# Performance work log

Measured on AMD Instinct MI355X. Metric: run time of the kernel, lower is better.

The kernel has to match this reference:

```python
import jax, jax.numpy as jnp
import numpy as np

DIM = 1024
HEADS = 16
DIM_HEAD = 64
INNER = HEADS * DIM_HEAD  # 1024
SCALE = DIM ** (-0.5)     # NOTE: source uses dim, not dim_head, for scaling


def setup_inputs() -> dict:
    key = jax.random.key(0)
    k_x, k_qkv, k_out = jax.random.split(key, 3)
    x = jax.random.normal(k_x, (4, 2048, DIM), dtype=jnp.float32)
    # store weights pre-transposed: y = x @ W  (equivalent to torch Linear with W.T)
    w_qkv = jax.random.normal(k_qkv, (DIM, 3 * INNER), dtype=jnp.float32) * 0.02
    w_out = jax.random.normal(k_out, (INNER, DIM), dtype=jnp.float32) * 0.02
    b_out = jnp.zeros((DIM,), dtype=jnp.float32)
    return {"x": x, "w_qkv": w_qkv, "w_out": w_out, "b_out": b_out}


def reference(x, w_qkv, w_out, b_out):
    b, n, _ = x.shape
    qkv = x @ w_qkv                                  # [b, n, 3*inner]
    q, k, v = jnp.split(qkv, 3, axis=-1)             # each [b, n, inner]

    def to_heads(t):
        return t.reshape(b, n, HEADS, DIM_HEAD).transpose(0, 2, 1, 3)  # [b, h, n, d]

    q, k, v = to_heads(q), to_heads(k), to_heads(v)
    dots = jnp.einsum("bhid,bhjd->bhij", q, k) * SCALE   # [b, h, n, n]
    attn = jax.nn.softmax(dots, axis=-1)
    out = jnp.einsum("bhij,bhjd->bhid", attn, v)         # [b, h, n, d]
    out = out.transpose(0, 2, 1, 3).reshape(b, n, INNER)  # [b, n, inner]
    return out @ w_out + b_out                            # dropout p=0 -> identity
```

## Files before the change

### kernel.cpp

```cpp
#include <hip/hip_runtime.h>
#include <math.h>

#define BATCH   4
#define NSEQ    2048
#define DIM     1024
#define HEADS   16
#define DHEAD   64
#define INNER   1024
#define MTOT    (BATCH*NSEQ)
#define SC_L2E  0.04508422f

typedef __attribute__((ext_vector_type(8))) unsigned short u16x8;
typedef __attribute__((ext_vector_type(4))) unsigned short u16x4;
typedef __attribute__((ext_vector_type(8))) short          bf16x8;
typedef __attribute__((ext_vector_type(4))) float          f32x4;

__device__ __forceinline__ unsigned short f2bf(float f) {
    unsigned int u = __builtin_bit_cast(unsigned int, f);
    u += 0x7FFFu + ((u >> 16) & 1u);
    return (unsigned short)(u >> 16);
}

__device__ __forceinline__ float fexp2(float x) {
    float r; asm("v_exp_f32 %0, %1" : "=v"(r) : "v"(x)); return r;
}

__device__ __forceinline__ unsigned int cvtpk(float lo, float hi) {
    unsigned int r; asm("v_cvt_pk_bf16_f32 %0, %1, %2" : "=v"(r) : "v"(lo), "v"(hi));
    return r;
}

#define GLDS16(gp, lp) __builtin_amdgcn_global_load_lds( \
    (const __attribute__((address_space(1))) unsigned int*)(gp), \
    (__attribute__((address_space(3))) unsigned int*)(lp), 16, 0, 0)

#define SWC(r, c) ((c) ^ (((r) & 7) << 3))

__global__ __launch_bounds__(256) void cvt_bf16(const float* __restrict__ in,
                                                unsigned short* __restrict__ out)
{
    const int i = blockIdx.x * 256 + threadIdx.x;
    const float4* p = reinterpret_cast<const float4*>(in) + (size_t)i * 2;
    float4 a = p[0], b = p[1];
    u16x8 o;
    o[0]=f2bf(a.x); o[1]=f2bf(a.y); o[2]=f2bf(a.z); o[3]=f2bf(a.w);
    o[4]=f2bf(b.x); o[5]=f2bf(b.y); o[6]=f2bf(b.z); o[7]=f2bf(b.w);
    reinterpret_cast<u16x8*>(out)[i] = o;
}

__global__ __launch_bounds__(256) void transp_bf16(const float* __restrict__ in,
                                                   unsigned short* __restrict__ out,
                                                   int R, int C)
{
    __shared__ float tile[32][33];
    const int c0 = blockIdx.x * 32, r0 = blockIdx.y * 32;
    const int tx = threadIdx.x & 31, ty = threadIdx.x >> 5;
#pragma unroll
    for (int i = 0; i < 32; i += 8)
        tile[ty + i][tx] = in[(size_t)(r0 + ty + i) * C + c0 + tx];
    __syncthreads();
#pragma unroll
    for (int i = 0; i < 32; i += 8)
        out[(size_t)(c0 + ty + i) * R + r0 + tx] = f2bf(tile[tx][ty + i]);
}


__global__ __launch_bounds__(256) void gemm_qkv_mfma(const unsigned short* __restrict__ A,
                                                     const unsigned short* __restrict__ Bt,
                                                     unsigned short* __restrict__ qb,
                                                     unsigned short* __restrict__ kb,
                                                     unsigned short* __restrict__ vt)
{
    __shared__ unsigned short As[128][32];
    __shared__ unsigned short Bs[128][32];

    const int t = threadIdx.x;
    const int l = t & 63, w = t >> 6;
    const int wr = w >> 1, wc = w & 1;
    const int g = l >> 4, ql = l & 15;
    const int row0 = blockIdx.y * 128;
    const int col0 = blockIdx.x * 128;
    const int lr = l >> 2, lc = l & 3;

    f32x4 acc[4][4];
#pragma unroll
    for (int mi = 0; mi < 4; ++mi)
#pragma unroll
        for (int ni = 0; ni < 4; ++ni)
#pragma unroll
            for (int r = 0; r < 4; ++r) acc[mi][ni][r] = 0.f;

    for (int k0 = 0; k0 < DIM; k0 += 32) {
        __syncthreads();
        {
            const unsigned short* ag = A  + (size_t)(row0 + 32 * w + lr) * DIM + k0 + lc * 8;
            const unsigned short* bg = Bt + (size_t)(col0 + 32 * w + lr) * DIM + k0 + lc * 8;
            GLDS16(ag,              &As[32 * w][0]);
            GLDS16(ag + 16 * DIM,   &As[32 * w + 16][0]);
            GLDS16(bg,              &Bs[32 * w][0]);
            GLDS16(bg + 16 * DIM,   &Bs[32 * w + 16][0]);
        }
        __syncthreads();

        bf16x8 af[4], bf[4];
#pragma unroll
        for (int mi = 0; mi < 4; ++mi)
            af[mi] = *reinterpret_cast<const bf16x8*>(&As[wr * 64 + mi * 16 + ql][g * 8]);
#pragma unroll
        for (int ni = 0; ni < 4; ++ni)
            bf[ni] = *reinterpret_cast<const bf16x8*>(&Bs[wc * 64 + ni * 16 + ql][g * 8]);
#pragma unroll
        for (int mi = 0; mi < 4; ++mi)
#pragma unroll
            for (int ni = 0; ni < 4; ++ni)
                acc[mi][ni] = __builtin_amdgcn_mfma_f32_16x16x32_bf16(af[mi], bf[ni], acc[mi][ni], 0, 0, 0);
    }

#pragma unroll
    for (int mi = 0; mi < 4; ++mi) {
        const int m0 = row0 + wr * 64 + mi * 16 + g * 4;
        const int b  = m0 >> 11, n0 = m0 & 2047;
#pragma unroll
        for (int ni = 0; ni < 4; ++ni) {
            const int c = col0 + wc * 64 + ni * 16 + ql;
            const int part = c >> 10, inner = c & 1023;
            const int h = inner >> 6, d = inner & 63;
            if (part == 2) {
                const int key0 = n0 & 63;
                const int nst  = (n0 & ~63)
                               | (key0 & 0x23)
                               | (((key0 >> 3) & 1) << 4)
                               | (((key0 >> 2) & 1) << 3)
                               | (((key0 >> 4) & 1) << 2);
                u16x4 pk;
#pragma unroll
                for (int r = 0; r < 4; ++r) pk[r] = f2bf(acc[mi][ni][r]);
                *reinterpret_cast<u16x4*>(&vt[(((size_t)b * HEADS + h) * DHEAD + d) * NSEQ + nst]) = pk;
            } else if (part == 0) {
                unsigned short* dst = qb + (((size_t)b * HEADS + h) * NSEQ + n0) * DHEAD + d;
#pragma unroll
                for (int r = 0; r < 4; ++r) dst[(size_t)r * DHEAD] = f2bf(acc[mi][ni][r] * SC_L2E);
            } else {
                unsigned short* dst = kb + (((size_t)b * HEADS + h) * NSEQ + n0) * DHEAD + d;
#pragma unroll
                for (int r = 0; r < 4; ++r) dst[(size_t)r * DHEAD] = f2bf(acc[mi][ni][r]);
            }
        }
    }
}

__global__ __launch_bounds__(256) void gemm_out_mfma(const unsigned short* __restrict__ A,
                                                     const unsigned short* __restrict__ Bt,
                                                     const float* __restrict__ bias,
                                                     float* __restrict__ out)
{
    __shared__ unsigned short As[128][32];
    __shared__ unsigned short Bs[128][32];

    const int t = threadIdx.x;
    const int l = t & 63, w = t >> 6;
    const int wr = w >> 1, wc = w & 1;
    const int g = l >> 4, ql = l & 15;
    const int row0 = blockIdx.y * 128;
    const int col0 = blockIdx.x * 128;
    const int lr = l >> 2, lc = l & 3;

    f32x4 acc[4][4];
#pragma unroll
    for (int mi = 0; mi < 4; ++mi)
#pragma unroll
        for (int ni = 0; ni < 4; ++ni)
#pragma unroll
            for (int r = 0; r < 4; ++r) acc[mi][ni][r] = 0.f;

    for (int k0 = 0; k0 < INNER; k0 += 32) {
        __syncthreads();
        {
            const unsigned short* ag = A  + (size_t)(row0 + 32 * w + lr) * INNER + k0 + lc * 8;
            const unsigned short* bg = Bt + (size_t)(col0 + 32 * w + lr) * INNER + k0 + lc * 8;
            GLDS16(ag,               &As[32 * w][0]);
            GLDS16(ag + 16 * INNER,  &As[32 * w + 16][0]);
            GLDS16(bg,               &Bs[32 * w][0]);
            GLDS16(bg + 16 * INNER,  &Bs[32 * w + 16][0]);
        }
        __syncthreads();

        bf16x8 af[4], bf[4];
#pragma unroll
        for (int mi = 0; mi < 4; ++mi)
            af[mi] = *reinterpret_cast<const bf16x8*>(&As[wr * 64 + mi * 16 + ql][g * 8]);
#pragma unroll
        for (int ni = 0; ni < 4; ++ni)
            bf[ni] = *reinterpret_cast<const bf16x8*>(&Bs[wc * 64 + ni * 16 + ql][g * 8]);
#pragma unroll
        for (int mi = 0; mi < 4; ++mi)
#pragma unroll
            for (int ni = 0; ni < 4; ++ni)
                acc[mi][ni] = __builtin_amdgcn_mfma_f32_16x16x32_bf16(af[mi], bf[ni], acc[mi][ni], 0, 0, 0);
    }

#pragma unroll
    for (int mi = 0; mi < 4; ++mi) {
        const int m0 = row0 + wr * 64 + mi * 16 + g * 4;
#pragma unroll
        for (int ni = 0; ni < 4; ++ni) {
            const int c = col0 + wc * 64 + ni * 16 + ql;
            const float bv = bias[c];
#pragma unroll
            for (int r = 0; r < 4; ++r)
                out[(size_t)(m0 + r) * DIM + c] = acc[mi][ni][r] + bv;
        }
    }
}

__global__ __launch_bounds__(512) void attn_mfma(const unsigned short* __restrict__ qg,
                                                 const unsigned short* __restrict__ kg,
                                                 const unsigned short* __restrict__ vtg,
                                                 unsigned short* __restrict__ og)
{
    __shared__ unsigned short Ks [2][64 * 64];
    __shared__ unsigned short Vts[2][64 * 64];

    const int bh = blockIdx.x;
    const int b = bh >> 4, h = bh & 15;
    const int qblk = blockIdx.y;
    const int t = threadIdx.x, l = t & 63, w = t >> 6;
    const int g = l >> 4, ql = l & 15;

    const size_t hb = (size_t)bh * NSEQ * DHEAD;

    bf16x8 qf[2][2];
#pragma unroll
    for (int qh = 0; qh < 2; ++qh) {
        const unsigned short* qrow = qg + hb + (size_t)(qblk * 256 + w * 32 + qh * 16 + ql) * DHEAD;
        qf[qh][0] = *reinterpret_cast<const bf16x8*>(qrow + g * 8);
        qf[qh][1] = *reinterpret_cast<const bf16x8*>(qrow + 32 + g * 8);
    }

    const int r = t >> 3, seg = t & 7;
    const unsigned short* kgp = kg  + hb + (size_t)r * DHEAD + seg * 8;
    const unsigned short* vgp = vtg + hb + (size_t)r * NSEQ  + seg * 8;
    const int st = r * 64 + ((seg ^ (r & 7)) * 8);

    {
        u16x8 k0 = *reinterpret_cast<const u16x8*>(kgp);
        u16x8 v0 = *reinterpret_cast<const u16x8*>(vgp);
        *reinterpret_cast<u16x8*>(&Ks [0][st]) = k0;
        *reinterpret_cast<u16x8*>(&Vts[0][st]) = v0;
    }
    __syncthreads();

    const unsigned short* kpre = kgp + 64 * DHEAD;
    const unsigned short* vpre = vgp + 64;

    f32x4 acc_o[2][4];
#pragma unroll
    for (int qh = 0; qh < 2; ++qh)
#pragma unroll
        for (int dt = 0; dt < 4; ++dt)
#pragma unroll
            for (int rr = 0; rr < 4; ++rr) acc_o[qh][dt][rr] = 0.f;
    float m_r[2] = {-INFINITY, -INFINITY};
    float l_r[2] = {0.f, 0.f};

    for (int kbi = 0; kbi < NSEQ / 64; ++kbi) {
        const int cur = kbi & 1;
        u16x8 nk, nv;
        const bool pre = (kbi + 1 < NSEQ / 64);
        if (pre) {
            nk = *reinterpret_cast<const u16x8*>(kpre);
            nv = *reinterpret_cast<const u16x8*>(vpre);
            kpre += 64 * DHEAD;
            vpre += 64;
        }

        f32x4 sacc[2][4];
#pragma unroll
        for (int qh = 0; qh < 2; ++qh)
#pragma unroll
            for (int jt = 0; jt < 4; ++jt)
#pragma unroll
                for (int rr = 0; rr < 4; ++rr) sacc[qh][jt][rr] = 0.f;
        __builtin_amdgcn_s_setprio(1);
#pragma unroll
        for (int jt = 0; jt < 4; ++jt) {
            const int row = jt * 16 + ql;
            bf16x8 kf0 = *reinterpret_cast<const bf16x8*>(&Ks[cur][row * 64 + SWC(row, g * 8)]);
            bf16x8 kf1 = *reinterpret_cast<const bf16x8*>(&Ks[cur][row * 64 + SWC(row, 32 + g * 8)]);
            sacc[0][jt] = __builtin_amdgcn_mfma_f32_16x16x32_bf16(kf0, qf[0][0], sacc[0][jt], 0, 0, 0);
            sacc[0][jt] = __builtin_amdgcn_mfma_f32_16x16x32_bf16(kf1, qf[0][1], sacc[0][jt], 0, 0, 0);
            sacc[1][jt] = __builtin_amdgcn_mfma_f32_16x16x32_bf16(kf0, qf[1][0], sacc[1][jt], 0, 0, 0);
            sacc[1][jt] = __builtin_amdgcn_mfma_f32_16x16x32_bf16(kf1, qf[1][1], sacc[1][jt], 0, 0, 0);
        }
        __builtin_amdgcn_s_setprio(0);

        bf16x8 pf[2][2];
#pragma unroll
        for (int qh = 0; qh < 2; ++qh) {
            float a0 = fmaxf(fmaxf(sacc[qh][0][0], sacc[qh][0][1]), sacc[qh][0][2]);
            float a1 = fmaxf(fmaxf(sacc[qh][0][3], sacc[qh][1][0]), sacc[qh][1][1]);
            float a2 = fmaxf(fmaxf(sacc[qh][1][2], sacc[qh][1][3]), sacc[qh][2][0]);
            float a3 = fmaxf(fmaxf(sacc[qh][2][1], sacc[qh][2][2]), sacc[qh][2][3]);
            float a4 = fmaxf(fmaxf(sacc[qh][3][0], sacc[qh][3][1]), sacc[qh][3][2]);
            float mx = fmaxf(fmaxf(fmaxf(a0, a1), a2), fmaxf(fmaxf(a3, a4), sacc[qh][3][3]));
            mx = fmaxf(mx, __shfl_xor(mx, 16));
            mx = fmaxf(mx, __shfl_xor(mx, 32));
            if (__any(mx > m_r[qh] + 8.f)) {
                const float m_new = fmaxf(m_r[qh], mx);
                const float alpha = fexp2(m_r[qh] - m_new);
                l_r[qh] *= alpha;
#pragma unroll
                for (int dt = 0; dt < 4; ++dt)
#pragma unroll
                    for (int rr = 0; rr < 4; ++rr) acc_o[qh][dt][rr] *= alpha;
                m_r[qh] = m_new;
            }
            float p[16];
#pragma unroll
            for (int jt = 0; jt < 4; ++jt)
#pragma unroll
                for (int rr = 0; rr < 4; ++rr)
                    p[jt * 4 + rr] = fexp2(sacc[qh][jt][rr] - m_r[qh]);
            float s0 = (p[0] + p[1]) + (p[2] + p[3]);
            float s1 = (p[4] + p[5]) + (p[6] + p[7]);
            float s2 = (p[8] + p[9]) + (p[10] + p[11]);
            float s3 = (p[12] + p[13]) + (p[14] + p[15]);
            float ps = (s0 + s1) + (s2 + s3);
            ps += __shfl_xor(ps, 16);
            ps += __shfl_xor(ps, 32);
            l_r[qh] += ps;

#pragma unroll
            for (int js = 0; js < 2; ++js) {
                unsigned int u0 = cvtpk(p[8 * js + 0], p[8 * js + 1]);
                unsigned int u1 = cvtpk(p[8 * js + 2], p[8 * js + 3]);
                unsigned int u2 = cvtpk(p[8 * js + 4], p[8 * js + 5]);
                unsigned int u3 = cvtpk(p[8 * js + 6], p[8 * js + 7]);
                uint4 uu = {u0, u1, u2, u3};
                pf[qh][js] = __builtin_bit_cast(bf16x8, uu);
            }
        }

        __builtin_amdgcn_s_setprio(1);
#pragma unroll
        for (int js = 0; js < 2; ++js) {
            bf16x8 vf[4];
#pragma unroll
            for (int dt = 0; dt < 4; ++dt) {
                const int row = dt * 16 + ql;
                vf[dt] = *reinterpret_cast<const bf16x8*>(&Vts[cur][row * 64 + SWC(row, js * 32 + g * 8)]);
            }
#pragma unroll
            for (int qh = 0; qh < 2; ++qh)
#pragma unroll
                for (int dt = 0; dt < 4; ++dt)
                    acc_o[qh][dt] = __builtin_amdgcn_mfma_f32_16x16x32_bf16(vf[dt], pf[qh][js], acc_o[qh][dt], 0, 0, 0);
        }
        __builtin_amdgcn_s_setprio(0);

        if (pre) {
            *reinterpret_cast<u16x8*>(&Ks [cur ^ 1][st]) = nk;
            *reinterpret_cast<u16x8*>(&Vts[cur ^ 1][st]) = nv;
        }
        __syncthreads();
    }

#pragma unroll
    for (int qh = 0; qh < 2; ++qh) {
        const float rinv = 1.0f / l_r[qh];
        const int n = qblk * 256 + w * 32 + qh * 16 + ql;
        unsigned short* dst = og + ((size_t)b * NSEQ + n) * INNER + h * DHEAD;
#pragma unroll
        for (int dt = 0; dt < 4; ++dt) {
            uint2 u;
            u.x = cvtpk(acc_o[qh][dt][0] * rinv, acc_o[qh][dt][1] * rinv);
            u.y = cvtpk(acc_o[qh][dt][2] * rinv, acc_o[qh][dt][3] * rinv);
            *reinterpret_cast<uint2*>(&dst[dt * 16 + g * 4]) = u;
        }
    }
}


extern "C" void kernel_launch(void* const* d_in, const int* in_sizes, int n_in,
                              void* d_out, int out_size, void* d_ws, size_t ws_size,
                              hipStream_t stream) {
    const float* x     = (const float*)d_in[0];
    const float* w_qkv = (const float*)d_in[1];
    const float* w_out = (const float*)d_in[2];
    const float* b_out = (const float*)d_in[3];
    float* out = (float*)d_out;

    unsigned short* ws = (unsigned short*)d_ws;
    const size_t nX  = (size_t)MTOT * DIM;
    const size_t nWq = (size_t)DIM * 3 * INNER;
    const size_t nWo = (size_t)DIM * INNER;
    unsigned short* Xb  = ws;
    unsigned short* Wqt = Xb  + nX;
    unsigned short* Wot = Wqt + nWq;
    unsigned short* qb  = Wot + nWo;
    unsigned short* kb  = qb  + nX;
    unsigned short* vt  = kb  + nX;
    unsigned short* Ob  = vt  + nX;

    cvt_bf16<<<dim3(nX / 8 / 256), dim3(256), 0, stream>>>(x, Xb);
    transp_bf16<<<dim3(3 * INNER / 32, DIM / 32), dim3(256), 0, stream>>>(w_qkv, Wqt, DIM, 3 * INNER);
    transp_bf16<<<dim3(DIM / 32, INNER / 32), dim3(256), 0, stream>>>(w_out, Wot, INNER, DIM);

    gemm_qkv_mfma<<<dim3(3 * INNER / 128, MTOT / 128), dim3(256), 0, stream>>>(Xb, Wqt, qb, kb, vt);
    attn_mfma<<<dim3(BATCH * HEADS, NSEQ / 256), dim3(512), 0, stream>>>(qb, kb, vt, Ob);
    gemm_out_mfma<<<dim3(DIM / 128, MTOT / 128), dim3(256), 0, stream>>>(Ob, Wot, b_out, out);
}
```

Baseline: 202.4 us.

## Rewrite QKV GEMM with 256x256 tiles, double-buffered LDS and phased MFMA scheduling

Replaces the 128x128 QKV projection GEMM with a 512-thread kernel that computes 256x256 output tiles over K-steps of 64. It double-buffers LDS, splits the next-tile global-to-LDS loads across the compute phases, and swizzles LDS addressing. MFMA bursts are wrapped in barriers with raised wave priority, a ping-pong style schedule meant to overlap memory traffic with matrix math and raise data reuse. The trade-offs are much larger LDS use (128 KB) and more accumulator registers, which lower occupancy. The grid also drops to 384 blocks, which may under-fill the GPU.

```diff
diff --git a/kernel.cpp b/kernel.cpp
--- a/kernel.cpp
+++ b/kernel.cpp
@@ -35,6 +35,8 @@
     (__attribute__((address_space(3))) unsigned int*)(lp), 16, 0, 0)
 
 #define SWC(r, c) ((c) ^ (((r) & 7) << 3))
+
+#define BAR() __builtin_amdgcn_s_barrier()
 
 __global__ __launch_bounds__(256) void cvt_bf16(const float* __restrict__ in,
                                                 unsigned short* __restrict__ out)
@@ -64,65 +66,177 @@
         out[(size_t)(c0 + ty + i) * R + r0 + tx] = f2bf(tile[tx][ty + i]);
 }
 
-
-__global__ __launch_bounds__(256) void gemm_qkv_mfma(const unsigned short* __restrict__ A,
-                                                     const unsigned short* __restrict__ Bt,
-                                                     unsigned short* __restrict__ qb,
-                                                     unsigned short* __restrict__ kb,
-                                                     unsigned short* __restrict__ vt)
+__global__ __launch_bounds__(512) void gemm_qkv_8p(const unsigned short* __restrict__ A,
+                                                   const unsigned short* __restrict__ Bt,
+                                                   unsigned short* __restrict__ qb,
+                                                   unsigned short* __restrict__ kb,
+                                                   unsigned short* __restrict__ vt)
 {
-    __shared__ unsigned short As[128][32];
-    __shared__ unsigned short Bs[128][32];
+    __shared__ unsigned short As[2][256 * 64];
+    __shared__ unsigned short Bs[2][256 * 64];
 
     const int t = threadIdx.x;
     const int l = t & 63, w = t >> 6;
-    const int wr = w >> 1, wc = w & 1;
+    const int wm = w >> 2, wn = w & 3;
     const int g = l >> 4, ql = l & 15;
-    const int row0 = blockIdx.y * 128;
-    const int col0 = blockIdx.x * 128;
-    const int lr = l >> 2, lc = l & 3;
-
-    f32x4 acc[4][4];
-#pragma unroll
-    for (int mi = 0; mi < 4; ++mi)
-#pragma unroll
-        for (int ni = 0; ni < 4; ++ni)
-#pragma unroll
-            for (int r = 0; r < 4; ++r) acc[mi][ni][r] = 0.f;
-
-    for (int k0 = 0; k0 < DIM; k0 += 32) {
-        __syncthreads();
+    const int row0 = blockIdx.y * 256;
+    const int col0 = blockIdx.x * 256;
+
+    const int lrow  = l >> 3;
+    const int lslot = (l & 7) ^ (lrow & 7);
+    const unsigned short* aSrc = A  + (size_t)(row0 + w * 32 + lrow) * DIM + lslot * 8;
+    const unsigned short* bSrc = Bt + (size_t)(col0 + w * 32 + lrow) * DIM + lslot * 8;
+
+    f32x4 acc[8][4];
+#pragma unroll
+    for (int mf = 0; mf < 8; ++mf)
+#pragma unroll
+        for (int nf = 0; nf < 4; ++nf)
+#pragma unroll
+            for (int r = 0; r < 4; ++r) acc[mf][nf][r] = 0.f;
+
+#pragma unroll
+    for (int i = 0; i < 4; ++i) {
+        GLDS16(aSrc + (size_t)i * 8 * DIM, &As[0][(w * 32 + i * 8) * 64]);
+        GLDS16(bSrc + (size_t)i * 8 * DIM, &Bs[0][(w * 32 + i * 8) * 64]);
+    }
+    asm volatile("s_waitcnt vmcnt(0)" ::: "memory");
+    __syncthreads();
+
+#pragma unroll 1
+    for (int kt = 0; kt < 16; ++kt) {
+        const int cur = kt & 1;
+        const int nxt = cur ^ 1;
+        const size_t nk0 = (size_t)(kt + 1) * 64;
+        const bool pre = (kt < 15);
+
+        bf16x8 bfc[4][2];
+
+        if (pre) {
+            GLDS16(aSrc + nk0,                   &As[nxt][(w * 32) * 64]);
+            GLDS16(aSrc + nk0 + (size_t)8 * DIM, &As[nxt][(w * 32 + 8) * 64]);
+            GLDS16(bSrc + nk0,                   &Bs[nxt][(w * 32) * 64]);
+            GLDS16(bSrc + nk0 + (size_t)8 * DIM, &Bs[nxt][(w * 32 + 8) * 64]);
+        }
+#pragma unroll
+        for (int nf = 0; nf < 4; ++nf) {
+            const int br = wn * 64 + nf * 16 + ql;
+#pragma unroll
+            for (int kh = 0; kh < 2; ++kh)
+                bfc[nf][kh] = *reinterpret_cast<const bf16x8*>(
+                    &Bs[cur][br * 64 + SWC(br, (kh * 4 + g) * 8)]);
+        }
         {
-            const unsigned short* ag = A  + (size_t)(row0 + 32 * w + lr) * DIM + k0 + lc * 8;
-            const unsigned short* bg = Bt + (size_t)(col0 + 32 * w + lr) * DIM + k0 + lc * 8;
-            GLDS16(ag,              &As[32 * w][0]);
-            GLDS16(ag + 16 * DIM,   &As[32 * w + 16][0]);
-            GLDS16(bg,              &Bs[32 * w][0]);
-            GLDS16(bg + 16 * DIM,   &Bs[32 * w + 16][0]);
-        }
-        __syncthreads();
-
-        bf16x8 af[4], bf[4];
-#pragma unroll
-        for (int mi = 0; mi < 4; ++mi)
-            af[mi] = *reinterpret_cast<const bf16x8*>(&As[wr * 64 + mi * 16 + ql][g * 8]);
-#pragma unroll
-        for (int ni = 0; ni < 4; ++ni)
-            bf[ni] = *reinterpret_cast<const bf16x8*>(&Bs[wc * 64 + ni * 16 + ql][g * 8]);
-#pragma unroll
-        for (int mi = 0; mi < 4; ++mi)
-#pragma unroll
-            for (int ni = 0; ni < 4; ++ni)
-                acc[mi][ni] = __builtin_amdgcn_mfma_f32_16x16x32_bf16(af[mi], bf[ni], acc[mi][ni], 0, 0, 0);
-    }
-
-#pragma unroll
-    for (int mi = 0; mi < 4; ++mi) {
-        const int m0 = row0 + wr * 64 + mi * 16 + g * 4;
+            bf16x8 af[2][2];
+#pragma unroll
+            for (int j = 0; j < 2; ++j) {
+                const int ar = wm * 128 + (0 + j) * 16 + ql;
+#pragma unroll
+                for (int kh = 0; kh < 2; ++kh)
+                    af[j][kh] = *reinterpret_cast<const bf16x8*>(
+                        &As[cur][ar * 64 + SWC(ar, (kh * 4 + g) * 8)]);
+            }
+            BAR();
+            __builtin_amdgcn_s_setprio(1);
+#pragma unroll
+            for (int j = 0; j < 2; ++j)
+#pragma unroll
+                for (int nf = 0; nf < 4; ++nf)
+#pragma unroll
+                    for (int kh = 0; kh < 2; ++kh)
+                        acc[0 + j][nf] = __builtin_amdgcn_mfma_f32_16x16x32_bf16(
+                            af[j][kh], bfc[nf][kh], acc[0 + j][nf], 0, 0, 0);
+            __builtin_amdgcn_s_setprio(0);
+            BAR();
+        }
+
+        if (pre) {
+            GLDS16(aSrc + nk0 + (size_t)16 * DIM, &As[nxt][(w * 32 + 16) * 64]);
+            GLDS16(aSrc + nk0 + (size_t)24 * DIM, &As[nxt][(w * 32 + 24) * 64]);
+            GLDS16(bSrc + nk0 + (size_t)16 * DIM, &Bs[nxt][(w * 32 + 16) * 64]);
+            GLDS16(bSrc + nk0 + (size_t)24 * DIM, &Bs[nxt][(w * 32 + 24) * 64]);
+        }
+        {
+            bf16x8 af[2][2];
+#pragma unroll
+            for (int j = 0; j < 2; ++j) {
+                const int ar = wm * 128 + (2 + j) * 16 + ql;
+#pragma unroll
+                for (int kh = 0; kh < 2; ++kh)
+                    af[j][kh] = *reinterpret_cast<const bf16x8*>(
+                        &As[cur][ar * 64 + SWC(ar, (kh * 4 + g) * 8)]);
+            }
+            BAR();
+            __builtin_amdgcn_s_setprio(1);
+#pragma unroll
+            for (int j = 0; j < 2; ++j)
+#pragma unroll
+                for (int nf = 0; nf < 4; ++nf)
+#pragma unroll
+                    for (int kh = 0; kh < 2; ++kh)
+                        acc[2 + j][nf] = __builtin_amdgcn_mfma_f32_16x16x32_bf16(
+                            af[j][kh], bfc[nf][kh], acc[2 + j][nf], 0, 0, 0);
+            __builtin_amdgcn_s_setprio(0);
+            BAR();
+        }
+
+        {
+            bf16x8 af[2][2];
+#pragma unroll
+            for (int j = 0; j < 2; ++j) {
+                const int ar = wm * 128 + (4 + j) * 16 + ql;
+#pragma unroll
+                for (int kh = 0; kh < 2; ++kh)
+                    af[j][kh] = *reinterpret_cast<const bf16x8*>(
+                        &As[cur][ar * 64 + SWC(ar, (kh * 4 + g) * 8)]);
+            }
+            BAR();
+            __builtin_amdgcn_s_setprio(1);
+#pragma unroll
+            for (int j = 0; j < 2; ++j)
+#pragma unroll
+                for (int nf = 0; nf < 4; ++nf)
+#pragma unroll
+                    for (int kh = 0; kh < 2; ++kh)
+                        acc[4 + j][nf] = __builtin_amdgcn_mfma_f32_16x16x32_bf16(
+                            af[j][kh], bfc[nf][kh], acc[4 + j][nf], 0, 0, 0);
+            __builtin_amdgcn_s_setprio(0);
+            BAR();
+        }
+
+        {
+            bf16x8 af[2][2];
+#pragma unroll
+            for (int j = 0; j < 2; ++j) {
+                const int ar = wm * 128 + (6 + j) * 16 + ql;
+#pragma unroll
+                for (int kh = 0; kh < 2; ++kh)
+                    af[j][kh] = *reinterpret_cast<const bf16x8*>(
+                        &As[cur][ar * 64 + SWC(ar, (kh * 4 + g) * 8)]);
+            }
+            BAR();
+            __builtin_amdgcn_s_setprio(1);
+#pragma unroll
+            for (int j = 0; j < 2; ++j)
+#pragma unroll
+                for (int nf = 0; nf < 4; ++nf)
+#pragma unroll
+                    for (int kh = 0; kh < 2; ++kh)
+                        acc[6 + j][nf] = __builtin_amdgcn_mfma_f32_16x16x32_bf16(
+                            af[j][kh], bfc[nf][kh], acc[6 + j][nf], 0, 0, 0);
+            __builtin_amdgcn_s_setprio(0);
+            asm volatile("s_waitcnt vmcnt(0)" ::: "memory");
+            BAR();
+        }
+    }
+
+#pragma unroll
+    for (int mf = 0; mf < 8; ++mf) {
+        const int m0 = row0 + wm * 128 + mf * 16 + g * 4;
         const int b  = m0 >> 11, n0 = m0 & 2047;
 #pragma unroll
-        for (int ni = 0; ni < 4; ++ni) {
-            const int c = col0 + wc * 64 + ni * 16 + ql;
+        for (int nf = 0; nf < 4; ++nf) {
+            const int c = col0 + wn * 64 + nf * 16 + ql;
             const int part = c >> 10, inner = c & 1023;
             const int h = inner >> 6, d = inner & 63;
             if (part == 2) {
@@ -134,16 +248,16 @@
                                | (((key0 >> 4) & 1) << 2);
                 u16x4 pk;
 #pragma unroll
-                for (int r = 0; r < 4; ++r) pk[r] = f2bf(acc[mi][ni][r]);
+                for (int r = 0; r < 4; ++r) pk[r] = f2bf(acc[mf][nf][r]);
                 *reinterpret_cast<u16x4*>(&vt[(((size_t)b * HEADS + h) * DHEAD + d) * NSEQ + nst]) = pk;
             } else if (part == 0) {
                 unsigned short* dst = qb + (((size_t)b * HEADS + h) * NSEQ + n0) * DHEAD + d;
 #pragma unroll
-                for (int r = 0; r < 4; ++r) dst[(size_t)r * DHEAD] = f2bf(acc[mi][ni][r] * SC_L2E);
+                for (int r = 0; r < 4; ++r) dst[(size_t)r * DHEAD] = f2bf(acc[mf][nf][r] * SC_L2E);
             } else {
                 unsigned short* dst = kb + (((size_t)b * HEADS + h) * NSEQ + n0) * DHEAD + d;
 #pragma unroll
-                for (int r = 0; r < 4; ++r) dst[(size_t)r * DHEAD] = f2bf(acc[mi][ni][r]);
+                for (int r = 0; r < 4; ++r) dst[(size_t)r * DHEAD] = f2bf(acc[mf][nf][r]);
             }
         }
     }
@@ -406,7 +520,7 @@
     transp_bf16<<<dim3(3 * INNER / 32, DIM / 32), dim3(256), 0, stream>>>(w_qkv, Wqt, DIM, 3 * INNER);
     transp_bf16<<<dim3(DIM / 32, INNER / 32), dim3(256), 0, stream>>>(w_out, Wot, INNER, DIM);
 
-    gemm_qkv_mfma<<<dim3(3 * INNER / 128, MTOT / 128), dim3(256), 0, stream>>>(Xb, Wqt, qb, kb, vt);
+    gemm_qkv_8p<<<dim3(3 * INNER / 256, MTOT / 256), dim3(512), 0, stream>>>(Xb, Wqt, qb, kb, vt);
     attn_mfma<<<dim3(BATCH * HEADS, NSEQ / 256), dim3(512), 0, stream>>>(qb, kb, vt, Ob);
     gemm_out_mfma<<<dim3(DIM / 128, MTOT / 128), dim3(256), 0, stream>>>(Ob, Wot, b_out, out);
 }
```

New measurement: 214.7 us. 1.06x slower.
